# Kernel tuning notes

Hardware: AMD Instinct MI355X
Metric: run time of the kernel (lower is better)

The kernel has to match this reference:

```python
import jax, jax.numpy as jnp
import numpy as np

B, T, F, D, HD = 16, 512, 16, 256, 256


def _init(k, shape, fan_in):
    return (jax.random.uniform(k, shape, minval=-1.0, maxval=1.0) / np.sqrt(fan_in)).astype(jnp.float32)


def setup_inputs() -> dict:
    key = jax.random.key(0)
    ks = jax.random.split(key, 16)
    return {
        "x": jax.random.normal(ks[0], (B, T, F), dtype=jnp.float32),
        # per-variable encoder params, batched over F (Linear(1,D) + GRN(D,HD,D))
        "w1": _init(ks[1], (F, D), 1), "b1": _init(ks[2], (F, D), 1),
        "fc1_w": _init(ks[3], (F, D, HD), D), "fc1_b": _init(ks[4], (F, HD), D),
        "fc2_w": _init(ks[5], (F, HD, D), HD), "fc2_b": _init(ks[6], (F, D), HD),
        "glu_w": _init(ks[7], (F, D, 2 * D), D), "glu_b": _init(ks[8], (F, 2 * D), D),
        "ln_g": jnp.ones((F, D), jnp.float32), "ln_b": jnp.zeros((F, D), jnp.float32),
        # weight GRN(F, HD, F); skip is Identity since d_in == d_out
        "wg_fc1_w": _init(ks[9], (F, HD), F), "wg_fc1_b": _init(ks[10], (HD,), F),
        "wg_fc2_w": _init(ks[11], (HD, F), HD), "wg_fc2_b": _init(ks[12], (F,), HD),
        "wg_glu_w": _init(ks[13], (F, 2 * F), F), "wg_glu_b": _init(ks[14], (2 * F,), F),
        "wg_ln_g": jnp.ones((F,), jnp.float32), "wg_ln_b": jnp.zeros((F,), jnp.float32),
    }


def _layernorm(x, g, b, eps=1e-5):
    m = jnp.mean(x, axis=-1, keepdims=True)
    v = jnp.var(x, axis=-1, keepdims=True)
    return (x - m) * jax.lax.rsqrt(v + eps) * g + b


def reference(x, w1, b1, fc1_w, fc1_b, fc2_w, fc2_b, glu_w, glu_b, ln_g, ln_b,
              wg_fc1_w, wg_fc1_b, wg_fc2_w, wg_fc2_b, wg_glu_w, wg_glu_b,
              wg_ln_g, wg_ln_b):
    # --- per-variable towers, batched over F (dropout is identity at eval) ---
    h0 = jax.nn.relu(x[..., None] * w1 + b1)                       # [B,T,F,D]
    y = jax.nn.elu(jnp.einsum('btfd,fdh->btfh', h0, fc1_w) + fc1_b)
    y = jnp.einsum('btfh,fhd->btfd', y, fc2_w) + fc2_b
    g = jnp.einsum('btfd,fde->btfe', y, glu_w) + glu_b             # [B,T,F,2D]
    a, gate = jnp.split(g, 2, axis=-1)
    H = _layernorm(h0 + a * jax.nn.sigmoid(gate), ln_g, ln_b)      # [B,T,F,D]
    # --- variable-weight GRN (time_distributed=True) ---
    yw = jax.nn.elu(x @ wg_fc1_w + wg_fc1_b)
    yw = yw @ wg_fc2_w + wg_fc2_b
    gw = x @ jnp.zeros((F, 0), x.dtype) if False else yw @ wg_glu_w + wg_glu_b
    aw, gatew = jnp.split(gw, 2, axis=-1)
    w = _layernorm(x + aw * jax.nn.sigmoid(gatew), wg_ln_g, wg_ln_b)
    w = jax.nn.softmax(w, axis=-1)                                 # [B,T,F]
    z = jnp.einsum('btfd,btf->btd', H, w)                          # [B,T,D]
    return z, w
```

## Files before the change

kernel.cpp:

```cpp
#include <hip/hip_runtime.h>
#include <hip/hip_bf16.h>

#define NBT 8192
#define NF  16
#define ND  256
#define NH  256
#define N2D 512

typedef short bf16x8 __attribute__((ext_vector_type(8)));
typedef float f32x4 __attribute__((ext_vector_type(4)));
typedef unsigned short u16x8 __attribute__((ext_vector_type(8)));

__device__ __forceinline__ float bf2f(unsigned short u) {
  return __uint_as_float(((unsigned)u) << 16);
}
__device__ __forceinline__ unsigned short f2bf(float f) {
  unsigned u = __float_as_uint(f);
  return (unsigned short)((u + 0x7FFFu + ((u >> 16) & 1u)) >> 16);
}

#define GLOAD16(src, dst)                                                     \
  __builtin_amdgcn_global_load_lds(                                           \
      (const __attribute__((address_space(1))) unsigned int*)(src),           \
      (__attribute__((address_space(3))) unsigned int*)(dst), 16, 0, 0)

__global__ __launch_bounds__(256) void wgrn_kernel(
    const float* __restrict__ x, const float* __restrict__ fw1,
    const float* __restrict__ fb1, const float* __restrict__ fw2,
    const float* __restrict__ fb2, const float* __restrict__ gwt,
    const float* __restrict__ gbt, const float* __restrict__ lng,
    const float* __restrict__ lnb, float* __restrict__ wout) {
  __shared__ float w1t[256 * 16];
  __shared__ float w2s[256 * 16];
  const int tid = threadIdx.x;
  for (int i = tid; i < 4096; i += 256) {
    int ff = i >> 8, j = i & 255;
    w1t[j * 16 + ff] = fw1[i];
    w2s[i] = fw2[i];
  }
  __syncthreads();
  const int sub  = tid & 7;
  const int rowi = tid >> 3;
  const int bt   = blockIdx.x * 32 + rowi;
  float xr[16];
#pragma unroll
  for (int i = 0; i < 4; ++i)
    *(float4*)&xr[i * 4] = *(const float4*)(x + (size_t)bt * 16 + i * 4);
  float acc2[16];
#pragma unroll
  for (int q = 0; q < 16; ++q) acc2[q] = 0.f;
  for (int j = sub; j < 256; j += 8) {
    float h = fb1[j];
    const float* wr = &w1t[j * 16];
#pragma unroll
    for (int q = 0; q < 16; ++q) h = fmaf(xr[q], wr[q], h);
    h = h > 0.f ? h : expm1f(h);
    const float* w2r = &w2s[j * 16];
#pragma unroll
    for (int q = 0; q < 16; ++q) acc2[q] = fmaf(h, w2r[q], acc2[q]);
  }
#pragma unroll
  for (int off = 1; off < 8; off <<= 1) {
#pragma unroll
    for (int q = 0; q < 16; ++q) acc2[q] += __shfl_xor(acc2[q], off);
  }
#pragma unroll
  for (int q = 0; q < 16; ++q) acc2[q] += fb2[q];
  float gw[32];
#pragma unroll
  for (int k = 0; k < 32; ++k) {
    float s = gbt[k];
#pragma unroll
    for (int q = 0; q < 16; ++q) s = fmaf(acc2[q], gwt[q * 32 + k], s);
    gw[k] = s;
  }
  float v[16];
  float mean = 0.f;
#pragma unroll
  for (int q = 0; q < 16; ++q) {
    float sg = 1.f / (1.f + __expf(-gw[16 + q]));
    v[q] = fmaf(gw[q], sg, xr[q]);
    mean += v[q];
  }
  mean *= (1.f / 16.f);
  float var = 0.f;
#pragma unroll
  for (int q = 0; q < 16; ++q) { float d = v[q] - mean; var = fmaf(d, d, var); }
  var *= (1.f / 16.f);
  float rstd = rsqrtf(var + 1e-5f);
  float mx = -1e30f;
#pragma unroll
  for (int q = 0; q < 16; ++q) {
    v[q] = (v[q] - mean) * rstd * lng[q] + lnb[q];
    mx = fmaxf(mx, v[q]);
  }
  float se = 0.f;
#pragma unroll
  for (int q = 0; q < 16; ++q) { v[q] = __expf(v[q] - mx); se += v[q]; }
  float inv = 1.f / se;
  if (sub == 0) {
#pragma unroll
    for (int i = 0; i < 4; ++i) {
      float4 o = { v[i*4+0]*inv, v[i*4+1]*inv, v[i*4+2]*inv, v[i*4+3]*inv };
      *(float4*)(wout + (size_t)bt * 16 + i * 4) = o;
    }
  }
}

__global__ void transpose_cast(const float* __restrict__ src,
                               unsigned short* __restrict__ dst, int K, int N) {
  __shared__ float tile[32][33];
  const int f = blockIdx.z;
  const float* s = src + (size_t)f * K * N;
  unsigned short* d = dst + (size_t)f * K * N;
  const int k0 = blockIdx.y * 32, n0 = blockIdx.x * 32;
  const int tx = threadIdx.x, ty = threadIdx.y;
#pragma unroll
  for (int i = 0; i < 32; i += 8)
    tile[ty + i][tx] = s[(size_t)(k0 + ty + i) * N + n0 + tx];
  __syncthreads();
#pragma unroll
  for (int i = 0; i < 32; i += 8)
    d[(size_t)(n0 + ty + i) * K + k0 + tx] = f2bf(tile[tx][ty + i]);
}

__global__ __launch_bounds__(256, 4) void g1_kernel(
    const float* __restrict__ x, const float* __restrict__ w1,
    const float* __restrict__ b1, const unsigned short* __restrict__ fc1t,
    const float* __restrict__ fc1_b, unsigned short* __restrict__ y1) {
  __shared__ __align__(16) char arena[34816];
  __shared__ float xw[128];
  unsigned short* abuf = (unsigned short*)arena;
  unsigned short* bbuf = (unsigned short*)(arena + 17408);
  unsigned short* cbuf = (unsigned short*)arena;
  const int tid = threadIdx.x, lane = tid & 63, wid = tid >> 6;
  const int rl = lane & 15, kc = lane >> 4;
  const int f = blockIdx.z, m0 = blockIdx.y * 128, n0 = blockIdx.x * 128;
  const unsigned short* Bf = fc1t + (size_t)f * NH * ND;
  const float* w1f = w1 + f * ND;
  const float* b1f = b1 + f * ND;
  if (tid < 128) xw[tid] = x[(size_t)(m0 + tid) * NF + f];
  const int wm = (wid >> 1) * 64, wn = (wid & 1) * 64;

  f32x4 acc[4][4];
#pragma unroll
  for (int m = 0; m < 4; ++m)
#pragma unroll
    for (int n = 0; n < 4; ++n) acc[m][n] = (f32x4){0.f, 0.f, 0.f, 0.f};

  for (int kt = 0; kt < ND; kt += 64) {
    __syncthreads();
#pragma unroll
    for (int i = 0; i < 4; ++i) {
      int s = tid + 256 * i;
      int row = s >> 3, sl = s & 7;
      const unsigned short* gb =
          Bf + (size_t)(n0 + row) * ND + kt + ((sl ^ (row & 7)) << 3);
      GLOAD16(gb, (char*)bbuf + (wid * 64 + 256 * i) * 16);
    }
#pragma unroll
    for (int i = 0; i < 4; ++i) {
      int vi = tid + 256 * i;
      int row = vi >> 3, c8 = vi & 7, c = kt + c8 * 8;
      float xv = xw[row];
      float4 wa = *(const float4*)(w1f + c);
      float4 wb = *(const float4*)(w1f + c + 4);
      float4 ba = *(const float4*)(b1f + c);
      float4 bb = *(const float4*)(b1f + c + 4);
      u16x8 o;
      o[0] = f2bf(fmaxf(fmaf(xv, wa.x, ba.x), 0.f));
      o[1] = f2bf(fmaxf(fmaf(xv, wa.y, ba.y), 0.f));
      o[2] = f2bf(fmaxf(fmaf(xv, wa.z, ba.z), 0.f));
      o[3] = f2bf(fmaxf(fmaf(xv, wa.w, ba.w), 0.f));
      o[4] = f2bf(fmaxf(fmaf(xv, wb.x, bb.x), 0.f));
      o[5] = f2bf(fmaxf(fmaf(xv, wb.y, bb.y), 0.f));
      o[6] = f2bf(fmaxf(fmaf(xv, wb.z, bb.z), 0.f));
      o[7] = f2bf(fmaxf(fmaf(xv, wb.w, bb.w), 0.f));
      *(u16x8*)(abuf + row * 68 + c8 * 8) = o;
    }
    __syncthreads();
#pragma unroll
    for (int kk = 0; kk < 2; ++kk) {
      bf16x8 av[4], bv[4];
      int s = kk * 4 + kc;
#pragma unroll
      for (int m = 0; m < 4; ++m) {
        int r = wm + m * 16 + rl;
        av[m] = *(const bf16x8*)(abuf + r * 68 + s * 8);
      }
#pragma unroll
      for (int n = 0; n < 4; ++n) {
        int rr = wn + n * 16 + rl;
        int ps = s ^ (rr & 7);
        bv[n] = *(const bf16x8*)((const char*)bbuf + rr * 128 + ps * 16);
      }
#pragma unroll
      for (int m = 0; m < 4; ++m)
#pragma unroll
        for (int n = 0; n < 4; ++n)
          acc[m][n] = __builtin_amdgcn_mfma_f32_16x16x32_bf16(av[m], bv[n],
                                                              acc[m][n], 0, 0, 0);
    }
  }

  __syncthreads();
  const int rq = lane >> 4;
#pragma unroll
  for (int n = 0; n < 4; ++n) {
    int cl = wn + n * 16 + rl;
    float bvv = fc1_b[f * NH + n0 + cl];
#pragma unroll
    for (int m = 0; m < 4; ++m) {
#pragma unroll
      for (int j = 0; j < 4; ++j) {
        int r = wm + m * 16 + rq * 4 + j;
        float v = acc[m][n][j] + bvv;
        v = v > 0.f ? v : expm1f(v);
        cbuf[r * 136 + cl] = f2bf(v);
      }
    }
  }
  __syncthreads();
#pragma unroll
  for (int v = 0; v < 8; ++v) {
    int row = (tid >> 4) + v * 16, chunk = tid & 15;
    u16x8 val = *(const u16x8*)(cbuf + row * 136 + chunk * 8);
    *(u16x8*)(y1 + ((size_t)f * NBT + m0 + row) * NH + n0 + chunk * 8) = val;
  }
}

__global__ __launch_bounds__(512, 4) void g2_kernel(
    const unsigned short* __restrict__ y1,
    const unsigned short* __restrict__ fc2t, const float* __restrict__ fc2_b,
    unsigned short* __restrict__ y2) {
  __shared__ __align__(16) char arena[49152];
  unsigned short* abuf = (unsigned short*)arena;
  unsigned short* bbuf = (unsigned short*)(arena + 16384);
  unsigned short* cbuf = (unsigned short*)arena;
  const int tid = threadIdx.x, lane = tid & 63, wid = tid >> 6;
  const int rl = lane & 15, kc = lane >> 4;
  const int f = blockIdx.y, m0 = blockIdx.x * 128;
  const unsigned short* Af = y1 + (size_t)f * NBT * NH;
  const unsigned short* Bf = fc2t + (size_t)f * ND * NH;
  const int wm = (wid >> 2) * 64, wn = (wid & 3) * 64;

  f32x4 acc[4][4];
#pragma unroll
  for (int m = 0; m < 4; ++m)
#pragma unroll
    for (int n = 0; n < 4; ++n) acc[m][n] = (f32x4){0.f, 0.f, 0.f, 0.f};

  for (int kt = 0; kt < NH; kt += 64) {
    __syncthreads();
#pragma unroll
    for (int i = 0; i < 2; ++i) {
      int s = tid + 512 * i;
      int row = s >> 3, sl = s & 7;
      const unsigned short* ga =
          Af + (size_t)(m0 + row) * NH + kt + ((sl ^ (row & 7)) << 3);
      GLOAD16(ga, (char*)abuf + (wid * 64 + 512 * i) * 16);
    }
#pragma unroll
    for (int i = 0; i < 4; ++i) {
      int s = tid + 512 * i;
      int row = s >> 3, sl = s & 7;
      const unsigned short* gb =
          Bf + (size_t)row * NH + kt + ((sl ^ (row & 7)) << 3);
      GLOAD16(gb, (char*)bbuf + (wid * 64 + 512 * i) * 16);
    }
    __syncthreads();
#pragma unroll
    for (int kk = 0; kk < 2; ++kk) {
      bf16x8 av[4], bv[4];
      int s = kk * 4 + kc;
#pragma unroll
      for (int m = 0; m < 4; ++m) {
        int r = wm + m * 16 + rl;
        int ps = s ^ (r & 7);
        av[m] = *(const bf16x8*)((const char*)abuf + r * 128 + ps * 16);
      }
#pragma unroll
      for (int n = 0; n < 4; ++n) {
        int rr = wn + n * 16 + rl;
        int ps = s ^ (rr & 7);
        bv[n] = *(const bf16x8*)((const char*)bbuf + rr * 128 + ps * 16);
      }
#pragma unroll
      for (int m = 0; m < 4; ++m)
#pragma unroll
        for (int n = 0; n < 4; ++n)
          acc[m][n] = __builtin_amdgcn_mfma_f32_16x16x32_bf16(av[m], bv[n],
                                                              acc[m][n], 0, 0, 0);
    }
  }

  const int rq = lane >> 4;
  const int hsel = (wid & 3) >> 1;
#pragma unroll
  for (int h = 0; h < 2; ++h) {
    __syncthreads();
    if (hsel == h) {
#pragma unroll
      for (int n = 0; n < 4; ++n) {
        int c = wn + n * 16 + rl;
        int cl = c - h * 128;
        float bvv = fc2_b[f * ND + c];
#pragma unroll
        for (int m = 0; m < 4; ++m) {
#pragma unroll
          for (int j = 0; j < 4; ++j) {
            int r = wm + m * 16 + rq * 4 + j;
            cbuf[r * 136 + cl] = f2bf(acc[m][n][j] + bvv);
          }
        }
      }
    }
    __syncthreads();
#pragma unroll
    for (int v = 0; v < 4; ++v) {
      int row = (tid >> 4) + v * 32, chunk = tid & 15;
      u16x8 val = *(const u16x8*)(cbuf + row * 136 + chunk * 8);
      *(u16x8*)(y2 + ((size_t)f * NBT + m0 + row) * ND + h * 128 + chunk * 8) =
          val;
    }
  }
}

__global__ __launch_bounds__(512, 4) void g3_kernel(
    const unsigned short* __restrict__ y2,
    const unsigned short* __restrict__ glut, const float* __restrict__ glu_b,
    const float* __restrict__ x, const float* __restrict__ w1,
    const float* __restrict__ b1, const float* __restrict__ ln_g,
    const float* __restrict__ ln_b, unsigned short* __restrict__ H) {
  __shared__ __align__(16) char arena[73728];
  __shared__ float xw[64];
  __shared__ float2 sums[8][64];
  __shared__ float2 sums2[64];
  unsigned short* abuf = (unsigned short*)arena;
  unsigned short* bbuf = (unsigned short*)(arena + 8192);
  unsigned short* vbuf = (unsigned short*)arena;

  const int tid = threadIdx.x, lane = tid & 63, wid = tid >> 6;
  const int rl = lane & 15, rq = lane >> 4;
  const int f = blockIdx.y, m0 = blockIdx.x * 64;
  const unsigned short* Af = y2 + (size_t)f * NBT * ND;
  const unsigned short* Bf = glut + (size_t)f * ND * N2D;
  const float* w1f = w1 + f * ND;
  const float* b1f = b1 + f * ND;
  const int colb = wid * 32;
  if (tid < 64) xw[tid] = x[(size_t)(m0 + tid) * NF + f];

  f32x4 acc[4][4];
#pragma unroll
  for (int m = 0; m < 4; ++m)
#pragma unroll
    for (int n = 0; n < 4; ++n) acc[m][n] = (f32x4){0.f, 0.f, 0.f, 0.f};

  for (int kt = 0; kt < ND; kt += 64) {
    __syncthreads();
    {
      int s = tid;
      int row = s >> 3, sl = s & 7;
      const unsigned short* ga =
          Af + (size_t)(m0 + row) * ND + kt + ((sl ^ (row & 7)) << 3);
      GLOAD16(ga, (char*)abuf + (wid * 64) * 16);
    }
#pragma unroll
    for (int i = 0; i < 8; ++i) {
      int s = tid + 512 * i;
      int row = s >> 3, sl = s & 7;
      const unsigned short* gb =
          Bf + (size_t)row * ND + kt + ((sl ^ (row & 7)) << 3);
      GLOAD16(gb, (char*)bbuf + (wid * 64 + 512 * i) * 16);
    }
    __syncthreads();
#pragma unroll
    for (int kk = 0; kk < 2; ++kk) {
      bf16x8 av[4], bv[4];
      int s = kk * 4 + rq;
#pragma unroll
      for (int m = 0; m < 4; ++m) {
        int r = m * 16 + rl;
        int ps = s ^ (r & 7);
        av[m] = *(const bf16x8*)((const char*)abuf + r * 128 + ps * 16);
      }
#pragma unroll
      for (int n = 0; n < 4; ++n) {
        int rr = (n < 2) ? (colb + n * 16 + rl)
                         : (256 + colb + (n - 2) * 16 + rl);
        int ps = s ^ (rr & 7);
        bv[n] = *(const bf16x8*)((const char*)bbuf + rr * 128 + ps * 16);
      }
#pragma unroll
      for (int m = 0; m < 4; ++m)
#pragma unroll
        for (int n = 0; n < 4; ++n)
          acc[m][n] = __builtin_amdgcn_mfma_f32_16x16x32_bf16(av[m], bv[n],
                                                              acc[m][n], 0, 0, 0);
    }
  }

#pragma unroll
  for (int n = 0; n < 2; ++n) {
    int cA = colb + n * 16 + rl;
    float ab_ = glu_b[f * N2D + cA];
    float gb_ = glu_b[f * N2D + 256 + cA];
    float w1c = w1f[cA], b1c = b1f[cA];
#pragma unroll
    for (int m = 0; m < 4; ++m) {
#pragma unroll
      for (int j = 0; j < 4; ++j) {
        int r = m * 16 + rq * 4 + j;
        float a = acc[m][n][j] + ab_;
        float g = acc[m][n + 2][j] + gb_;
        float sg = 1.f / (1.f + __expf(-g));
        float h0 = fmaxf(fmaf(xw[r], w1c, b1c), 0.f);
        acc[m][n][j] = fmaf(a, sg, h0);
      }
    }
  }
#pragma unroll
  for (int m = 0; m < 4; ++m) {
#pragma unroll
    for (int j = 0; j < 4; ++j) {
      float s = acc[m][0][j] + acc[m][1][j];
      float q = fmaf(acc[m][0][j], acc[m][0][j],
                     acc[m][1][j] * acc[m][1][j]);
#pragma unroll
      for (int off = 1; off < 16; off <<= 1) {
        s += __shfl_xor(s, off);
        q += __shfl_xor(q, off);
      }
      if (rl == 0) sums[wid][m * 16 + rq * 4 + j] = make_float2(s, q);
    }
  }
  __syncthreads();
  if (tid < 64) {
    float tot = 0.f, tot2 = 0.f;
#pragma unroll
    for (int wv = 0; wv < 8; ++wv) {
      float2 p = sums[wv][tid];
      tot += p.x;
      tot2 += p.y;
    }
    float mean = tot * (1.f / 256.f);
    float var  = tot2 * (1.f / 256.f) - mean * mean;
    sums2[tid] = make_float2(mean, rsqrtf(var + 1e-5f));
  }
  __syncthreads();
#pragma unroll
  for (int n = 0; n < 2; ++n) {
    int cA = colb + n * 16 + rl;
    float lg = ln_g[f * ND + cA], lb = ln_b[f * ND + cA];
#pragma unroll
    for (int m = 0; m < 4; ++m) {
#pragma unroll
      for (int j = 0; j < 4; ++j) {
        int r = m * 16 + rq * 4 + j;
        float2 mr = sums2[r];
        vbuf[r * 264 + cA] = f2bf(fmaf((acc[m][n][j] - mr.x) * mr.y, lg, lb));
      }
    }
  }
  __syncthreads();
  {
    int row = tid >> 3, chunk = tid & 7;
    unsigned short* Hrow = H + ((size_t)f * NBT + m0 + row) * ND;
#pragma unroll
    for (int v = 0; v < 4; ++v) {
      u16x8 val = *(const u16x8*)(vbuf + row * 264 + chunk * 8 + v * 64);
      *(u16x8*)(Hrow + chunk * 8 + v * 64) = val;
    }
  }
}

__global__ __launch_bounds__(256) void combine_kernel(
    const unsigned short* __restrict__ H, const float* __restrict__ w,
    float* __restrict__ z) {
  int idx = blockIdx.x * 256 + threadIdx.x;
  int bt = idx >> 5;
  int d  = (idx & 31) << 3;
  float a[8];
#pragma unroll
  for (int j = 0; j < 8; ++j) a[j] = 0.f;
#pragma unroll
  for (int f = 0; f < 16; ++f) {
    u16x8 hv = *(const u16x8*)(H + ((size_t)f * NBT + bt) * ND + d);
    float wvv = w[bt * 16 + f];
#pragma unroll
    for (int j = 0; j < 8; ++j) a[j] = fmaf(bf2f(hv[j]), wvv, a[j]);
  }
  float4 o0 = {a[0], a[1], a[2], a[3]};
  float4 o1 = {a[4], a[5], a[6], a[7]};
  *(float4*)(z + (size_t)bt * ND + d)     = o0;
  *(float4*)(z + (size_t)bt * ND + d + 4) = o1;
}

extern "C" void kernel_launch(void* const* d_in, const int* in_sizes, int n_in,
                              void* d_out, int out_size, void* d_ws,
                              size_t ws_size, hipStream_t stream) {
  const float* x        = (const float*)d_in[0];
  const float* w1       = (const float*)d_in[1];
  const float* b1       = (const float*)d_in[2];
  const float* fc1_w    = (const float*)d_in[3];
  const float* fc1_b    = (const float*)d_in[4];
  const float* fc2_w    = (const float*)d_in[5];
  const float* fc2_b    = (const float*)d_in[6];
  const float* glu_w    = (const float*)d_in[7];
  const float* glu_b    = (const float*)d_in[8];
  const float* ln_g     = (const float*)d_in[9];
  const float* ln_b     = (const float*)d_in[10];
  const float* wg_fc1_w = (const float*)d_in[11];
  const float* wg_fc1_b = (const float*)d_in[12];
  const float* wg_fc2_w = (const float*)d_in[13];
  const float* wg_fc2_b = (const float*)d_in[14];
  const float* wg_glu_w = (const float*)d_in[15];
  const float* wg_glu_b = (const float*)d_in[16];
  const float* wg_ln_g  = (const float*)d_in[17];
  const float* wg_ln_b  = (const float*)d_in[18];

  char* ws = (char*)d_ws;
  unsigned short* fc1t = (unsigned short*)ws;
  unsigned short* fc2t = fc1t + (size_t)NF * NH * ND;
  unsigned short* glut = fc2t + (size_t)NF * ND * NH;
  unsigned short* y1   = (unsigned short*)(ws + (8ull << 20));
  unsigned short* y2   = (unsigned short*)(ws + (72ull << 20));
  unsigned short* Hbuf = (unsigned short*)(ws + (136ull << 20));

  float* zout = (float*)d_out;
  float* wout = zout + (size_t)NBT * ND;

  wgrn_kernel<<<256, 256, 0, stream>>>(x, wg_fc1_w, wg_fc1_b, wg_fc2_w,
                                       wg_fc2_b, wg_glu_w, wg_glu_b, wg_ln_g,
                                       wg_ln_b, wout);
  transpose_cast<<<dim3(8, 8, NF),  dim3(32, 8), 0, stream>>>(fc1_w, fc1t, ND, NH);
  transpose_cast<<<dim3(8, 8, NF),  dim3(32, 8), 0, stream>>>(fc2_w, fc2t, NH, ND);
  transpose_cast<<<dim3(16, 8, NF), dim3(32, 8), 0, stream>>>(glu_w, glut, ND, N2D);

  g1_kernel<<<dim3(NH / 128, NBT / 128, NF), 256, 0, stream>>>(
      x, w1, b1, fc1t, fc1_b, y1);
  g2_kernel<<<dim3(NBT / 128, NF), 512, 0, stream>>>(y1, fc2t, fc2_b, y2);
  g3_kernel<<<dim3(NBT / 64, NF), 512, 0, stream>>>(y2, glut, glu_b, x, w1, b1,
                                                    ln_g, ln_b, Hbuf);
  combine_kernel<<<(NBT * ND / 8) / 256, 256, 0, stream>>>(Hbuf, wout, zout);

  (void)in_sizes; (void)n_in; (void)out_size; (void)ws_size;
}
```

Measured before the change: 232.1 us.

## Keep per-variable weights in registers and loop over row tiles in GEMM kernels

The three per-variable GEMM kernels are restructured so each wave loads its slice of the weight matrix once into registers (full K of 256) and then loops over several 64-row tiles. A operands are read directly from global memory, or built in LDS for the h0 tile in g1, instead of being staged with global_load_lds double tiles. The grids shrink to 512/512/256 blocks and occupancy hints drop to 2. The three transpose-cast launches are merged into one. This trades LDS staging and repeated weight reloads for much higher register pressure and uncoalesced direct global A loads, with less parallelism.

```diff
diff --git a/kernel.cpp b/kernel.cpp
--- a/kernel.cpp
+++ b/kernel.cpp
@@ -18,11 +18,6 @@
   unsigned u = __float_as_uint(f);
   return (unsigned short)((u + 0x7FFFu + ((u >> 16) & 1u)) >> 16);
 }
-
-#define GLOAD16(src, dst)                                                     \
-  __builtin_amdgcn_global_load_lds(                                           \
-      (const __attribute__((address_space(1))) unsigned int*)(src),           \
-      (__attribute__((address_space(3))) unsigned int*)(dst), 16, 0, 0)
 
 __global__ __launch_bounds__(256) void wgrn_kernel(
     const float* __restrict__ x, const float* __restrict__ fw1,
@@ -107,13 +102,26 @@
   }
 }
 
-__global__ void transpose_cast(const float* __restrict__ src,
-                               unsigned short* __restrict__ dst, int K, int N) {
+__global__ void transpose_all(const float* __restrict__ fc1_w,
+                              const float* __restrict__ fc2_w,
+                              const float* __restrict__ glu_w,
+                              unsigned short* __restrict__ fc1t,
+                              unsigned short* __restrict__ fc2t,
+                              unsigned short* __restrict__ glut) {
   __shared__ float tile[32][33];
-  const int f = blockIdx.z;
+  const int which = blockIdx.z >> 4;
+  const int f     = blockIdx.z & 15;
+  const float* src;
+  unsigned short* dst;
+  int K, N, bx = blockIdx.x;
+  if (which == 0)      { src = fc1_w; dst = fc1t; K = ND; N = NH; }
+  else if (which == 1) { src = fc2_w; dst = fc2t; K = NH; N = ND; }
+  else                 { src = glu_w; dst = glut; K = ND; N = N2D;
+                         bx += (which == 3) ? 8 : 0; }
+  if (bx * 32 >= N) return;
   const float* s = src + (size_t)f * K * N;
   unsigned short* d = dst + (size_t)f * K * N;
-  const int k0 = blockIdx.y * 32, n0 = blockIdx.x * 32;
+  const int k0 = blockIdx.y * 32, n0 = bx * 32;
   const int tx = threadIdx.x, ty = threadIdx.y;
 #pragma unroll
   for (int i = 0; i < 32; i += 8)
@@ -124,352 +132,293 @@
     d[(size_t)(n0 + ty + i) * K + k0 + tx] = f2bf(tile[tx][ty + i]);
 }
 
-__global__ __launch_bounds__(256, 4) void g1_kernel(
+__global__ __launch_bounds__(256, 2) void g1_kernel(
     const float* __restrict__ x, const float* __restrict__ w1,
     const float* __restrict__ b1, const unsigned short* __restrict__ fc1t,
     const float* __restrict__ fc1_b, unsigned short* __restrict__ y1) {
-  __shared__ __align__(16) char arena[34816];
-  __shared__ float xw[128];
-  unsigned short* abuf = (unsigned short*)arena;
-  unsigned short* bbuf = (unsigned short*)(arena + 17408);
-  unsigned short* cbuf = (unsigned short*)arena;
+  __shared__ __align__(16) unsigned short h0buf[64 * 264];
+  __shared__ __align__(16) unsigned short cbuf[64 * 264];
   const int tid = threadIdx.x, lane = tid & 63, wid = tid >> 6;
   const int rl = lane & 15, kc = lane >> 4;
-  const int f = blockIdx.z, m0 = blockIdx.y * 128, n0 = blockIdx.x * 128;
+  const int f = blockIdx.y;
   const unsigned short* Bf = fc1t + (size_t)f * NH * ND;
   const float* w1f = w1 + f * ND;
   const float* b1f = b1 + f * ND;
-  if (tid < 128) xw[tid] = x[(size_t)(m0 + tid) * NF + f];
-  const int wm = (wid >> 1) * 64, wn = (wid & 1) * 64;
-
-  f32x4 acc[4][4];
-#pragma unroll
-  for (int m = 0; m < 4; ++m)
-#pragma unroll
-    for (int n = 0; n < 4; ++n) acc[m][n] = (f32x4){0.f, 0.f, 0.f, 0.f};
-
-  for (int kt = 0; kt < ND; kt += 64) {
-    __syncthreads();
-#pragma unroll
-    for (int i = 0; i < 4; ++i) {
-      int s = tid + 256 * i;
-      int row = s >> 3, sl = s & 7;
-      const unsigned short* gb =
-          Bf + (size_t)(n0 + row) * ND + kt + ((sl ^ (row & 7)) << 3);
-      GLOAD16(gb, (char*)bbuf + (wid * 64 + 256 * i) * 16);
-    }
-#pragma unroll
-    for (int i = 0; i < 4; ++i) {
-      int vi = tid + 256 * i;
-      int row = vi >> 3, c8 = vi & 7, c = kt + c8 * 8;
-      float xv = xw[row];
-      float4 wa = *(const float4*)(w1f + c);
-      float4 wb = *(const float4*)(w1f + c + 4);
-      float4 ba = *(const float4*)(b1f + c);
-      float4 bb = *(const float4*)(b1f + c + 4);
+  const int wn = wid * 64;
+
+  bf16x8 bfrag[4][8];
+#pragma unroll
+  for (int n = 0; n < 4; ++n)
+#pragma unroll
+    for (int kt = 0; kt < 8; ++kt)
+      bfrag[n][kt] = *(const bf16x8*)(Bf + (size_t)(wn + n * 16 + rl) * ND +
+                                      kt * 32 + kc * 8);
+  float bias[4];
+#pragma unroll
+  for (int n = 0; n < 4; ++n) bias[n] = fc1_b[f * NH + wn + n * 16 + rl];
+
+  const int cc = (tid & 31) * 8;
+  const float4 wva = *(const float4*)(w1f + cc);
+  const float4 wvb = *(const float4*)(w1f + cc + 4);
+  const float4 bva = *(const float4*)(b1f + cc);
+  const float4 bvb = *(const float4*)(b1f + cc + 4);
+
+  for (int t = 0; t < 4; ++t) {
+    const int m0 = (blockIdx.x * 4 + t) * 64;
+    __syncthreads();
+#pragma unroll
+    for (int i = 0; i < 8; ++i) {
+      int row = (tid >> 5) + i * 8;
+      float xv = x[(size_t)(m0 + row) * NF + f];
       u16x8 o;
-      o[0] = f2bf(fmaxf(fmaf(xv, wa.x, ba.x), 0.f));
-      o[1] = f2bf(fmaxf(fmaf(xv, wa.y, ba.y), 0.f));
-      o[2] = f2bf(fmaxf(fmaf(xv, wa.z, ba.z), 0.f));
-      o[3] = f2bf(fmaxf(fmaf(xv, wa.w, ba.w), 0.f));
-      o[4] = f2bf(fmaxf(fmaf(xv, wb.x, bb.x), 0.f));
-      o[5] = f2bf(fmaxf(fmaf(xv, wb.y, bb.y), 0.f));
-      o[6] = f2bf(fmaxf(fmaf(xv, wb.z, bb.z), 0.f));
-      o[7] = f2bf(fmaxf(fmaf(xv, wb.w, bb.w), 0.f));
-      *(u16x8*)(abuf + row * 68 + c8 * 8) = o;
-    }
-    __syncthreads();
-#pragma unroll
-    for (int kk = 0; kk < 2; ++kk) {
-      bf16x8 av[4], bv[4];
-      int s = kk * 4 + kc;
-#pragma unroll
-      for (int m = 0; m < 4; ++m) {
-        int r = wm + m * 16 + rl;
-        av[m] = *(const bf16x8*)(abuf + r * 68 + s * 8);
-      }
-#pragma unroll
-      for (int n = 0; n < 4; ++n) {
-        int rr = wn + n * 16 + rl;
-        int ps = s ^ (rr & 7);
-        bv[n] = *(const bf16x8*)((const char*)bbuf + rr * 128 + ps * 16);
-      }
+      o[0] = f2bf(fmaxf(fmaf(xv, wva.x, bva.x), 0.f));
+      o[1] = f2bf(fmaxf(fmaf(xv, wva.y, bva.y), 0.f));
+      o[2] = f2bf(fmaxf(fmaf(xv, wva.z, bva.z), 0.f));
+      o[3] = f2bf(fmaxf(fmaf(xv, wva.w, bva.w), 0.f));
+      o[4] = f2bf(fmaxf(fmaf(xv, wvb.x, bvb.x), 0.f));
+      o[5] = f2bf(fmaxf(fmaf(xv, wvb.y, bvb.y), 0.f));
+      o[6] = f2bf(fmaxf(fmaf(xv, wvb.z, bvb.z), 0.f));
+      o[7] = f2bf(fmaxf(fmaf(xv, wvb.w, bvb.w), 0.f));
+      *(u16x8*)(h0buf + row * 264 + cc) = o;
+    }
+    __syncthreads();
+
+    f32x4 acc[4][4];
+#pragma unroll
+    for (int m = 0; m < 4; ++m)
+#pragma unroll
+      for (int n = 0; n < 4; ++n) acc[m][n] = (f32x4){0.f, 0.f, 0.f, 0.f};
+#pragma unroll
+    for (int kt = 0; kt < 8; ++kt) {
+      bf16x8 av[4];
+#pragma unroll
+      for (int m = 0; m < 4; ++m)
+        av[m] = *(const bf16x8*)(h0buf + (m * 16 + rl) * 264 + kt * 32 + kc * 8);
 #pragma unroll
       for (int m = 0; m < 4; ++m)
 #pragma unroll
         for (int n = 0; n < 4; ++n)
-          acc[m][n] = __builtin_amdgcn_mfma_f32_16x16x32_bf16(av[m], bv[n],
-                                                              acc[m][n], 0, 0, 0);
-    }
-  }
-
-  __syncthreads();
-  const int rq = lane >> 4;
-#pragma unroll
-  for (int n = 0; n < 4; ++n) {
-    int cl = wn + n * 16 + rl;
-    float bvv = fc1_b[f * NH + n0 + cl];
-#pragma unroll
-    for (int m = 0; m < 4; ++m) {
-#pragma unroll
-      for (int j = 0; j < 4; ++j) {
-        int r = wm + m * 16 + rq * 4 + j;
-        float v = acc[m][n][j] + bvv;
-        v = v > 0.f ? v : expm1f(v);
-        cbuf[r * 136 + cl] = f2bf(v);
-      }
-    }
-  }
-  __syncthreads();
-#pragma unroll
-  for (int v = 0; v < 8; ++v) {
-    int row = (tid >> 4) + v * 16, chunk = tid & 15;
-    u16x8 val = *(const u16x8*)(cbuf + row * 136 + chunk * 8);
-    *(u16x8*)(y1 + ((size_t)f * NBT + m0 + row) * NH + n0 + chunk * 8) = val;
-  }
-}
-
-__global__ __launch_bounds__(512, 4) void g2_kernel(
+          acc[m][n] = __builtin_amdgcn_mfma_f32_16x16x32_bf16(
+              av[m], bfrag[n][kt], acc[m][n], 0, 0, 0);
+    }
+
+#pragma unroll
+    for (int n = 0; n < 4; ++n) {
+      int c = wn + n * 16 + rl;
+#pragma unroll
+      for (int m = 0; m < 4; ++m)
+#pragma unroll
+        for (int j = 0; j < 4; ++j) {
+          int r = m * 16 + kc * 4 + j;
+          float v = acc[m][n][j] + bias[n];
+          v = v > 0.f ? v : expm1f(v);
+          cbuf[r * 264 + c] = f2bf(v);
+        }
+    }
+    __syncthreads();
+#pragma unroll
+    for (int v = 0; v < 8; ++v) {
+      int job = tid + 256 * v;
+      int row = job >> 5, ch = job & 31;
+      u16x8 val = *(const u16x8*)(cbuf + row * 264 + ch * 8);
+      *(u16x8*)(y1 + ((size_t)f * NBT + m0 + row) * NH + ch * 8) = val;
+    }
+  }
+}
+
+__global__ __launch_bounds__(256, 2) void g2_kernel(
     const unsigned short* __restrict__ y1,
     const unsigned short* __restrict__ fc2t, const float* __restrict__ fc2_b,
     unsigned short* __restrict__ y2) {
-  __shared__ __align__(16) char arena[49152];
-  unsigned short* abuf = (unsigned short*)arena;
-  unsigned short* bbuf = (unsigned short*)(arena + 16384);
-  unsigned short* cbuf = (unsigned short*)arena;
+  __shared__ __align__(16) unsigned short cbuf[64 * 264];
   const int tid = threadIdx.x, lane = tid & 63, wid = tid >> 6;
   const int rl = lane & 15, kc = lane >> 4;
-  const int f = blockIdx.y, m0 = blockIdx.x * 128;
-  const unsigned short* Af = y1 + (size_t)f * NBT * NH;
+  const int f = blockIdx.y;
   const unsigned short* Bf = fc2t + (size_t)f * ND * NH;
-  const int wm = (wid >> 2) * 64, wn = (wid & 3) * 64;
-
-  f32x4 acc[4][4];
-#pragma unroll
-  for (int m = 0; m < 4; ++m)
-#pragma unroll
-    for (int n = 0; n < 4; ++n) acc[m][n] = (f32x4){0.f, 0.f, 0.f, 0.f};
-
-  for (int kt = 0; kt < NH; kt += 64) {
-    __syncthreads();
-#pragma unroll
-    for (int i = 0; i < 2; ++i) {
-      int s = tid + 512 * i;
-      int row = s >> 3, sl = s & 7;
-      const unsigned short* ga =
-          Af + (size_t)(m0 + row) * NH + kt + ((sl ^ (row & 7)) << 3);
-      GLOAD16(ga, (char*)abuf + (wid * 64 + 512 * i) * 16);
-    }
-#pragma unroll
-    for (int i = 0; i < 4; ++i) {
-      int s = tid + 512 * i;
-      int row = s >> 3, sl = s & 7;
-      const unsigned short* gb =
-          Bf + (size_t)row * NH + kt + ((sl ^ (row & 7)) << 3);
-      GLOAD16(gb, (char*)bbuf + (wid * 64 + 512 * i) * 16);
-    }
-    __syncthreads();
-#pragma unroll
-    for (int kk = 0; kk < 2; ++kk) {
-      bf16x8 av[4], bv[4];
-      int s = kk * 4 + kc;
-#pragma unroll
-      for (int m = 0; m < 4; ++m) {
-        int r = wm + m * 16 + rl;
-        int ps = s ^ (r & 7);
-        av[m] = *(const bf16x8*)((const char*)abuf + r * 128 + ps * 16);
-      }
-#pragma unroll
-      for (int n = 0; n < 4; ++n) {
-        int rr = wn + n * 16 + rl;
-        int ps = s ^ (rr & 7);
-        bv[n] = *(const bf16x8*)((const char*)bbuf + rr * 128 + ps * 16);
-      }
+  const int wn = wid * 64;
+
+  bf16x8 bfrag[4][8];
+#pragma unroll
+  for (int n = 0; n < 4; ++n)
+#pragma unroll
+    for (int kt = 0; kt < 8; ++kt)
+      bfrag[n][kt] = *(const bf16x8*)(Bf + (size_t)(wn + n * 16 + rl) * NH +
+                                      kt * 32 + kc * 8);
+  float bias[4];
+#pragma unroll
+  for (int n = 0; n < 4; ++n) bias[n] = fc2_b[f * ND + wn + n * 16 + rl];
+
+  for (int t = 0; t < 4; ++t) {
+    const int m0 = (blockIdx.x * 4 + t) * 64;
+    const unsigned short* Ag = y1 + ((size_t)f * NBT + m0) * NH;
+    f32x4 acc[4][4];
+#pragma unroll
+    for (int m = 0; m < 4; ++m)
+#pragma unroll
+      for (int n = 0; n < 4; ++n) acc[m][n] = (f32x4){0.f, 0.f, 0.f, 0.f};
+#pragma unroll
+    for (int kt = 0; kt < 8; ++kt) {
+      bf16x8 av[4];
+#pragma unroll
+      for (int m = 0; m < 4; ++m)
+        av[m] = *(const bf16x8*)(Ag + (size_t)(m * 16 + rl) * NH + kt * 32 +
+                                 kc * 8);
 #pragma unroll
       for (int m = 0; m < 4; ++m)
 #pragma unroll
         for (int n = 0; n < 4; ++n)
-          acc[m][n] = __builtin_amdgcn_mfma_f32_16x16x32_bf16(av[m], bv[n],
-                                                              acc[m][n], 0, 0, 0);
-    }
-  }
-
-  const int rq = lane >> 4;
-  const int hsel = (wid & 3) >> 1;
-#pragma unroll
-  for (int h = 0; h < 2; ++h) {
-    __syncthreads();
-    if (hsel == h) {
-#pragma unroll
-      for (int n = 0; n < 4; ++n) {
-        int c = wn + n * 16 + rl;
-        int cl = c - h * 128;
-        float bvv = fc2_b[f * ND + c];
-#pragma unroll
-        for (int m = 0; m < 4; ++m) {
-#pragma unroll
-          for (int j = 0; j < 4; ++j) {
-            int r = wm + m * 16 + rq * 4 + j;
-            cbuf[r * 136 + cl] = f2bf(acc[m][n][j] + bvv);
-          }
+          acc[m][n] = __builtin_amdgcn_mfma_f32_16x16x32_bf16(
+              av[m], bfrag[n][kt], acc[m][n], 0, 0, 0);
+    }
+    if (t) __syncthreads();
+#pragma unroll
+    for (int n = 0; n < 4; ++n) {
+      int c = wn + n * 16 + rl;
+#pragma unroll
+      for (int m = 0; m < 4; ++m)
+#pragma unroll
+        for (int j = 0; j < 4; ++j) {
+          int r = m * 16 + kc * 4 + j;
+          cbuf[r * 264 + c] = f2bf(acc[m][n][j] + bias[n]);
         }
-      }
-    }
-    __syncthreads();
-#pragma unroll
-    for (int v = 0; v < 4; ++v) {
-      int row = (tid >> 4) + v * 32, chunk = tid & 15;
-      u16x8 val = *(const u16x8*)(cbuf + row * 136 + chunk * 8);
-      *(u16x8*)(y2 + ((size_t)f * NBT + m0 + row) * ND + h * 128 + chunk * 8) =
-          val;
-    }
-  }
-}
-
-__global__ __launch_bounds__(512, 4) void g3_kernel(
+    }
+    __syncthreads();
+#pragma unroll
+    for (int v = 0; v < 8; ++v) {
+      int job = tid + 256 * v;
+      int row = job >> 5, ch = job & 31;
+      u16x8 val = *(const u16x8*)(cbuf + row * 264 + ch * 8);
+      *(u16x8*)(y2 + ((size_t)f * NBT + m0 + row) * ND + ch * 8) = val;
+    }
+  }
+}
+
+__global__ __launch_bounds__(512, 2) void g3_kernel(
     const unsigned short* __restrict__ y2,
     const unsigned short* __restrict__ glut, const float* __restrict__ glu_b,
     const float* __restrict__ x, const float* __restrict__ w1,
     const float* __restrict__ b1, const float* __restrict__ ln_g,
     const float* __restrict__ ln_b, unsigned short* __restrict__ H) {
-  __shared__ __align__(16) char arena[73728];
   __shared__ float xw[64];
   __shared__ float2 sums[8][64];
   __shared__ float2 sums2[64];
-  unsigned short* abuf = (unsigned short*)arena;
-  unsigned short* bbuf = (unsigned short*)(arena + 8192);
-  unsigned short* vbuf = (unsigned short*)arena;
-
+  __shared__ __align__(16) unsigned short vbuf[64 * 264];
   const int tid = threadIdx.x, lane = tid & 63, wid = tid >> 6;
   const int rl = lane & 15, rq = lane >> 4;
-  const int f = blockIdx.y, m0 = blockIdx.x * 64;
-  const unsigned short* Af = y2 + (size_t)f * NBT * ND;
+  const int f = blockIdx.y;
   const unsigned short* Bf = glut + (size_t)f * ND * N2D;
-  const float* w1f = w1 + f * ND;
-  const float* b1f = b1 + f * ND;
   const int colb = wid * 32;
-  if (tid < 64) xw[tid] = x[(size_t)(m0 + tid) * NF + f];
-
-  f32x4 acc[4][4];
-#pragma unroll
-  for (int m = 0; m < 4; ++m)
-#pragma unroll
-    for (int n = 0; n < 4; ++n) acc[m][n] = (f32x4){0.f, 0.f, 0.f, 0.f};
-
-  for (int kt = 0; kt < ND; kt += 64) {
-    __syncthreads();
-    {
-      int s = tid;
-      int row = s >> 3, sl = s & 7;
-      const unsigned short* ga =
-          Af + (size_t)(m0 + row) * ND + kt + ((sl ^ (row & 7)) << 3);
-      GLOAD16(ga, (char*)abuf + (wid * 64) * 16);
-    }
-#pragma unroll
-    for (int i = 0; i < 8; ++i) {
-      int s = tid + 512 * i;
-      int row = s >> 3, sl = s & 7;
-      const unsigned short* gb =
-          Bf + (size_t)row * ND + kt + ((sl ^ (row & 7)) << 3);
-      GLOAD16(gb, (char*)bbuf + (wid * 64 + 512 * i) * 16);
-    }
-    __syncthreads();
-#pragma unroll
-    for (int kk = 0; kk < 2; ++kk) {
-      bf16x8 av[4], bv[4];
-      int s = kk * 4 + rq;
-#pragma unroll
-      for (int m = 0; m < 4; ++m) {
-        int r = m * 16 + rl;
-        int ps = s ^ (r & 7);
-        av[m] = *(const bf16x8*)((const char*)abuf + r * 128 + ps * 16);
-      }
-#pragma unroll
-      for (int n = 0; n < 4; ++n) {
-        int rr = (n < 2) ? (colb + n * 16 + rl)
-                         : (256 + colb + (n - 2) * 16 + rl);
-        int ps = s ^ (rr & 7);
-        bv[n] = *(const bf16x8*)((const char*)bbuf + rr * 128 + ps * 16);
-      }
-#pragma unroll
-      for (int m = 0; m < 4; ++m)
-#pragma unroll
-        for (int n = 0; n < 4; ++n)
-          acc[m][n] = __builtin_amdgcn_mfma_f32_16x16x32_bf16(av[m], bv[n],
-                                                              acc[m][n], 0, 0, 0);
-    }
-  }
-
+
+  bf16x8 bfrag[4][8];
+#pragma unroll
+  for (int n = 0; n < 4; ++n) {
+    int brow = (n < 2) ? (colb + n * 16 + rl) : (256 + colb + (n - 2) * 16 + rl);
+#pragma unroll
+    for (int kt = 0; kt < 8; ++kt)
+      bfrag[n][kt] =
+          *(const bf16x8*)(Bf + (size_t)brow * ND + kt * 32 + rq * 8);
+  }
+  float w1c[2], b1c[2], ab_[2], gb_[2], lg[2], lb[2];
 #pragma unroll
   for (int n = 0; n < 2; ++n) {
     int cA = colb + n * 16 + rl;
-    float ab_ = glu_b[f * N2D + cA];
-    float gb_ = glu_b[f * N2D + 256 + cA];
-    float w1c = w1f[cA], b1c = b1f[cA];
+    w1c[n] = w1[f * ND + cA];
+    b1c[n] = b1[f * ND + cA];
+    ab_[n] = glu_b[f * N2D + cA];
+    gb_[n] = glu_b[f * N2D + 256 + cA];
+    lg[n] = ln_g[f * ND + cA];
+    lb[n] = ln_b[f * ND + cA];
+  }
+
+  for (int t = 0; t < 8; ++t) {
+    const int m0 = (blockIdx.x * 8 + t) * 64;
+    if (tid < 64) xw[tid] = x[(size_t)(m0 + tid) * NF + f];
+    __syncthreads();
+    const unsigned short* Ag = y2 + ((size_t)f * NBT + m0) * ND;
+    f32x4 acc[4][4];
+#pragma unroll
+    for (int m = 0; m < 4; ++m)
+#pragma unroll
+      for (int n = 0; n < 4; ++n) acc[m][n] = (f32x4){0.f, 0.f, 0.f, 0.f};
+#pragma unroll
+    for (int kt = 0; kt < 8; ++kt) {
+      bf16x8 av[4];
+#pragma unroll
+      for (int m = 0; m < 4; ++m)
+        av[m] = *(const bf16x8*)(Ag + (size_t)(m * 16 + rl) * ND + kt * 32 +
+                                 rq * 8);
+#pragma unroll
+      for (int m = 0; m < 4; ++m)
+#pragma unroll
+        for (int n = 0; n < 4; ++n)
+          acc[m][n] = __builtin_amdgcn_mfma_f32_16x16x32_bf16(
+              av[m], bfrag[n][kt], acc[m][n], 0, 0, 0);
+    }
+#pragma unroll
+    for (int n = 0; n < 2; ++n) {
+#pragma unroll
+      for (int m = 0; m < 4; ++m) {
+#pragma unroll
+        for (int j = 0; j < 4; ++j) {
+          int r = m * 16 + rq * 4 + j;
+          float a = acc[m][n][j] + ab_[n];
+          float g = acc[m][n + 2][j] + gb_[n];
+          float sg = 1.f / (1.f + __expf(-g));
+          float h0 = fmaxf(fmaf(xw[r], w1c[n], b1c[n]), 0.f);
+          acc[m][n][j] = fmaf(a, sg, h0);
+        }
+      }
+    }
 #pragma unroll
     for (int m = 0; m < 4; ++m) {
 #pragma unroll
       for (int j = 0; j < 4; ++j) {
-        int r = m * 16 + rq * 4 + j;
-        float a = acc[m][n][j] + ab_;
-        float g = acc[m][n + 2][j] + gb_;
-        float sg = 1.f / (1.f + __expf(-g));
-        float h0 = fmaxf(fmaf(xw[r], w1c, b1c), 0.f);
-        acc[m][n][j] = fmaf(a, sg, h0);
+        float s = acc[m][0][j] + acc[m][1][j];
+        float q = fmaf(acc[m][0][j], acc[m][0][j],
+                       acc[m][1][j] * acc[m][1][j]);
+#pragma unroll
+        for (int off = 1; off < 16; off <<= 1) {
+          s += __shfl_xor(s, off);
+          q += __shfl_xor(q, off);
+        }
+        if (rl == 0) sums[wid][m * 16 + rq * 4 + j] = make_float2(s, q);
       }
     }
-  }
-#pragma unroll
-  for (int m = 0; m < 4; ++m) {
-#pragma unroll
-    for (int j = 0; j < 4; ++j) {
-      float s = acc[m][0][j] + acc[m][1][j];
-      float q = fmaf(acc[m][0][j], acc[m][0][j],
-                     acc[m][1][j] * acc[m][1][j]);
-#pragma unroll
-      for (int off = 1; off < 16; off <<= 1) {
-        s += __shfl_xor(s, off);
-        q += __shfl_xor(q, off);
+    __syncthreads();
+    if (tid < 64) {
+      float tot = 0.f, tot2 = 0.f;
+#pragma unroll
+      for (int wv = 0; wv < 8; ++wv) {
+        float2 p = sums[wv][tid];
+        tot += p.x;
+        tot2 += p.y;
       }
-      if (rl == 0) sums[wid][m * 16 + rq * 4 + j] = make_float2(s, q);
-    }
-  }
-  __syncthreads();
-  if (tid < 64) {
-    float tot = 0.f, tot2 = 0.f;
-#pragma unroll
-    for (int wv = 0; wv < 8; ++wv) {
-      float2 p = sums[wv][tid];
-      tot += p.x;
-      tot2 += p.y;
-    }
-    float mean = tot * (1.f / 256.f);
-    float var  = tot2 * (1.f / 256.f) - mean * mean;
-    sums2[tid] = make_float2(mean, rsqrtf(var + 1e-5f));
-  }
-  __syncthreads();
-#pragma unroll
-  for (int n = 0; n < 2; ++n) {
-    int cA = colb + n * 16 + rl;
-    float lg = ln_g[f * ND + cA], lb = ln_b[f * ND + cA];
-#pragma unroll
-    for (int m = 0; m < 4; ++m) {
-#pragma unroll
-      for (int j = 0; j < 4; ++j) {
-        int r = m * 16 + rq * 4 + j;
-        float2 mr = sums2[r];
-        vbuf[r * 264 + cA] = f2bf(fmaf((acc[m][n][j] - mr.x) * mr.y, lg, lb));
+      float mean = tot * (1.f / 256.f);
+      float var  = tot2 * (1.f / 256.f) - mean * mean;
+      sums2[tid] = make_float2(mean, rsqrtf(var + 1e-5f));
+    }
+    __syncthreads();
+#pragma unroll
+    for (int n = 0; n < 2; ++n) {
+      int cA = colb + n * 16 + rl;
+#pragma unroll
+      for (int m = 0; m < 4; ++m) {
+#pragma unroll
+        for (int j = 0; j < 4; ++j) {
+          int r = m * 16 + rq * 4 + j;
+          float2 mr = sums2[r];
+          vbuf[r * 264 + cA] =
+              f2bf(fmaf((acc[m][n][j] - mr.x) * mr.y, lg[n], lb[n]));
+        }
       }
     }
-  }
-  __syncthreads();
-  {
-    int row = tid >> 3, chunk = tid & 7;
-    unsigned short* Hrow = H + ((size_t)f * NBT + m0 + row) * ND;
+    __syncthreads();
 #pragma unroll
     for (int v = 0; v < 4; ++v) {
-      u16x8 val = *(const u16x8*)(vbuf + row * 264 + chunk * 8 + v * 64);
-      *(u16x8*)(Hrow + chunk * 8 + v * 64) = val;
+      int job = tid + 512 * v;
+      int row = job >> 5, ch = job & 31;
+      u16x8 val = *(const u16x8*)(vbuf + row * 264 + ch * 8);
+      *(u16x8*)(H + ((size_t)f * NBT + m0 + row) * ND + ch * 8) = val;
     }
   }
 }
@@ -533,15 +482,13 @@
   wgrn_kernel<<<256, 256, 0, stream>>>(x, wg_fc1_w, wg_fc1_b, wg_fc2_w,
                                        wg_fc2_b, wg_glu_w, wg_glu_b, wg_ln_g,
                                        wg_ln_b, wout);
-  transpose_cast<<<dim3(8, 8, NF),  dim3(32, 8), 0, stream>>>(fc1_w, fc1t, ND, NH);
-  transpose_cast<<<dim3(8, 8, NF),  dim3(32, 8), 0, stream>>>(fc2_w, fc2t, NH, ND);
-  transpose_cast<<<dim3(16, 8, NF), dim3(32, 8), 0, stream>>>(glu_w, glut, ND, N2D);
-
-  g1_kernel<<<dim3(NH / 128, NBT / 128, NF), 256, 0, stream>>>(
-      x, w1, b1, fc1t, fc1_b, y1);
-  g2_kernel<<<dim3(NBT / 128, NF), 512, 0, stream>>>(y1, fc2t, fc2_b, y2);
-  g3_kernel<<<dim3(NBT / 64, NF), 512, 0, stream>>>(y2, glut, glu_b, x, w1, b1,
-                                                    ln_g, ln_b, Hbuf);
+  transpose_all<<<dim3(16, 8, 64), dim3(32, 8), 0, stream>>>(
+      fc1_w, fc2_w, glu_w, fc1t, fc2t, glut);
+
+  g1_kernel<<<dim3(32, 16), 256, 0, stream>>>(x, w1, b1, fc1t, fc1_b, y1);
+  g2_kernel<<<dim3(32, 16), 256, 0, stream>>>(y1, fc2t, fc2_b, y2);
+  g3_kernel<<<dim3(16, 16), 512, 0, stream>>>(y2, glut, glu_b, x, w1, b1,
+                                              ln_g, ln_b, Hbuf);
   combine_kernel<<<(NBT * ND / 8) / 256, 256, 0, stream>>>(Hbuf, wout, zout);
 
   (void)in_sizes; (void)n_in; (void)out_size; (void)ws_size;
```

After: 273.0 us. +17.6%, slower.

## Remap GEMM blocks per XCD for L2 locality and merge weight transposes

Applied to the files above, without the earlier changes.

Block indices in the three GEMM kernels are remapped so that each group of eight consecutively dispatched blocks is spread across the XCDs in a way that gives each XCD a contiguous range of logical tiles. Each XCD then works mostly on the same feature's weights and neighbouring activation rows, which should improve L2 reuse. The three weight transpose-cast launches are merged into one launch with early-exit blocks; some glu tiles are written twice with identical values. The g2 epilogue barrier is also restructured slightly.

```diff
diff --git a/kernel.cpp b/kernel.cpp
--- a/kernel.cpp
+++ b/kernel.cpp
@@ -107,13 +107,26 @@
   }
 }
 
-__global__ void transpose_cast(const float* __restrict__ src,
-                               unsigned short* __restrict__ dst, int K, int N) {
+__global__ void transpose_all(const float* __restrict__ fc1_w,
+                              const float* __restrict__ fc2_w,
+                              const float* __restrict__ glu_w,
+                              unsigned short* __restrict__ fc1t,
+                              unsigned short* __restrict__ fc2t,
+                              unsigned short* __restrict__ glut) {
   __shared__ float tile[32][33];
-  const int f = blockIdx.z;
+  const int which = blockIdx.z >> 4;
+  const int f     = blockIdx.z & 15;
+  const float* src;
+  unsigned short* dst;
+  int K, N, bx = blockIdx.x;
+  if (which == 0)      { src = fc1_w; dst = fc1t; K = ND; N = NH; }
+  else if (which == 1) { src = fc2_w; dst = fc2t; K = NH; N = ND; }
+  else                 { src = glu_w; dst = glut; K = ND; N = N2D;
+                         bx += (which == 3) ? 8 : 0; }
+  if (bx * 32 >= N) return;
   const float* s = src + (size_t)f * K * N;
   unsigned short* d = dst + (size_t)f * K * N;
-  const int k0 = blockIdx.y * 32, n0 = blockIdx.x * 32;
+  const int k0 = blockIdx.y * 32, n0 = bx * 32;
   const int tx = threadIdx.x, ty = threadIdx.y;
 #pragma unroll
   for (int i = 0; i < 32; i += 8)
@@ -135,7 +148,9 @@
   unsigned short* cbuf = (unsigned short*)arena;
   const int tid = threadIdx.x, lane = tid & 63, wid = tid >> 6;
   const int rl = lane & 15, kc = lane >> 4;
-  const int f = blockIdx.z, m0 = blockIdx.y * 128, n0 = blockIdx.x * 128;
+  int hb = blockIdx.x + 2 * (blockIdx.y + 64 * blockIdx.z);
+  int L  = (hb & 7) * 256 + (hb >> 3);
+  const int f = L >> 7, m0 = ((L >> 1) & 63) * 128, n0 = (L & 1) * 128;
   const unsigned short* Bf = fc1t + (size_t)f * NH * ND;
   const float* w1f = w1 + f * ND;
   const float* b1f = b1 + f * ND;
@@ -239,7 +254,9 @@
   unsigned short* cbuf = (unsigned short*)arena;
   const int tid = threadIdx.x, lane = tid & 63, wid = tid >> 6;
   const int rl = lane & 15, kc = lane >> 4;
-  const int f = blockIdx.y, m0 = blockIdx.x * 128;
+  int hb = blockIdx.x + 64 * blockIdx.y;
+  int L  = (hb & 7) * 128 + (hb >> 3);
+  const int f = L >> 6, m0 = (L & 63) * 128;
   const unsigned short* Af = y1 + (size_t)f * NBT * NH;
   const unsigned short* Bf = fc2t + (size_t)f * ND * NH;
   const int wm = (wid >> 2) * 64, wn = (wid & 3) * 64;
@@ -294,11 +311,12 @@
     }
   }
 
+  __syncthreads();
   const int rq = lane >> 4;
   const int hsel = (wid & 3) >> 1;
 #pragma unroll
   for (int h = 0; h < 2; ++h) {
-    __syncthreads();
+    if (h) __syncthreads();
     if (hsel == h) {
 #pragma unroll
       for (int n = 0; n < 4; ++n) {
@@ -342,7 +360,9 @@
 
   const int tid = threadIdx.x, lane = tid & 63, wid = tid >> 6;
   const int rl = lane & 15, rq = lane >> 4;
-  const int f = blockIdx.y, m0 = blockIdx.x * 64;
+  int hb = blockIdx.x + 128 * blockIdx.y;
+  int L  = (hb & 7) * 256 + (hb >> 3);
+  const int f = L >> 7, m0 = (L & 127) * 64;
   const unsigned short* Af = y2 + (size_t)f * NBT * ND;
   const unsigned short* Bf = glut + (size_t)f * ND * N2D;
   const float* w1f = w1 + f * ND;
@@ -533,9 +553,8 @@
   wgrn_kernel<<<256, 256, 0, stream>>>(x, wg_fc1_w, wg_fc1_b, wg_fc2_w,
                                        wg_fc2_b, wg_glu_w, wg_glu_b, wg_ln_g,
                                        wg_ln_b, wout);
-  transpose_cast<<<dim3(8, 8, NF),  dim3(32, 8), 0, stream>>>(fc1_w, fc1t, ND, NH);
-  transpose_cast<<<dim3(8, 8, NF),  dim3(32, 8), 0, stream>>>(fc2_w, fc2t, NH, ND);
-  transpose_cast<<<dim3(16, 8, NF), dim3(32, 8), 0, stream>>>(glu_w, glut, ND, N2D);
+  transpose_all<<<dim3(16, 8, 64), dim3(32, 8), 0, stream>>>(
+      fc1_w, fc2_w, glu_w, fc1t, fc2t, glut);
 
   g1_kernel<<<dim3(NH / 128, NBT / 128, NF), 256, 0, stream>>>(
       x, w1, b1, fc1t, fc1_b, y1);
```

Result: faster. 227.0 us (-2.2%).
